# Kernel optimization log

Measured on AMD Instinct MI355X. Metric: run time of the kernel, lower is better.

Reference implementation:

```python
import jax, jax.numpy as jnp
import numpy as np

B, S, D_IN = 2, 2048, 2048
H, G, HD = 16, 4, 128          # num_heads, num_kv_groups, head_dim
GROUP = H // G                  # 4 query heads per kv group
D_OUT = H * HD                  # 2048
EPS = 1e-6


def _rope_tables(seq_len, head_dim, theta=10000.0):
    inv = 1.0 / (theta ** (np.arange(0, head_dim, 2, dtype=np.float32) / head_dim))
    pos = np.arange(seq_len, dtype=np.float32)
    ang = np.outer(pos, inv)                      # [S, HD/2]
    ang = np.concatenate([ang, ang], axis=-1)     # [S, HD]
    return jnp.asarray(np.cos(ang)), jnp.asarray(np.sin(ang))


def setup_inputs() -> dict:
    key = jax.random.key(0)
    ks = jax.random.split(key, 6)
    x = jax.random.normal(ks[0], (B, S, D_IN), dtype=jnp.float32)
    # Linear weights stored as [in, out] so y = x @ W (same math as nn.Linear)
    Wq = jax.random.normal(ks[1], (D_IN, 2 * D_OUT), dtype=jnp.float32) * (D_IN ** -0.5)
    Wk = jax.random.normal(ks[2], (D_IN, G * HD), dtype=jnp.float32) * (D_IN ** -0.5)
    Wv = jax.random.normal(ks[3], (D_IN, G * HD), dtype=jnp.float32) * (D_IN ** -0.5)
    Wo = jax.random.normal(ks[4], (D_OUT, D_IN), dtype=jnp.float32) * (D_OUT ** -0.5)
    q_norm_w = jnp.zeros((HD,), dtype=jnp.float32)  # Qwen-style zero-init (scale = 1 + w)
    k_norm_w = jnp.zeros((HD,), dtype=jnp.float32)
    cos, sin = _rope_tables(S, HD)
    mask = jnp.triu(jnp.ones((S, S), dtype=bool), k=1)  # causal: True above diagonal is masked
    return {"x": x, "Wq": Wq, "Wk": Wk, "Wv": Wv, "Wo": Wo,
            "q_norm_w": q_norm_w, "k_norm_w": k_norm_w,
            "cos": cos, "sin": sin, "mask": mask}


def _rmsnorm(x, w):
    xf = x.astype(jnp.float32)
    n = xf * jax.lax.rsqrt(jnp.mean(xf * xf, axis=-1, keepdims=True) + EPS)
    return (n * (1.0 + w.astype(jnp.float32))).astype(x.dtype)


def _apply_rope(x, cos, sin):
    # x: [..., S, HD]; full-dim rotation (rot_dim == head_dim)
    s = x.shape[-2]
    c = cos[:s][None, None]
    sn = sin[:s][None, None]
    x1, x2 = x[..., : HD // 2], x[..., HD // 2 :]
    rotated = jnp.concatenate([-x2, x1], axis=-1)
    return (x * c + rotated * sn).astype(x.dtype)


def reference(x, Wq, Wk, Wv, Wo, q_norm_w, k_norm_w, cos, sin, mask):
    b, s, _ = x.shape
    qg = (x @ Wq).reshape(b, s, H, 2 * HD)
    q, gate = qg[..., :HD], qg[..., HD:]
    gate = gate.reshape(b, s, D_OUT)
    q = q.transpose(0, 2, 1, 3)                                 # [b,H,s,HD]
    k = (x @ Wk).reshape(b, s, G, HD).transpose(0, 2, 1, 3)     # [b,G,s,HD]
    v = (x @ Wv).reshape(b, s, G, HD).transpose(0, 2, 1, 3)
    q = _rmsnorm(q, q_norm_w)
    k = _rmsnorm(k, k_norm_w)
    q = _apply_rope(q, cos, sin)
    k = _apply_rope(k, cos, sin)
    # GQA: group query heads by kv group instead of repeat_interleave on k/v
    qg4 = q.reshape(b, G, GROUP, s, HD)
    scores = jnp.einsum("bgjqd,bgkd->bgjqk", qg4, k)            # [b,G,GROUP,s,s]
    scores = jnp.where(mask[None, None, None], -jnp.inf, scores)
    w = jax.nn.softmax((scores * (HD ** -0.5)).astype(jnp.float32), axis=-1).astype(q.dtype)
    ctx = jnp.einsum("bgjqk,bgkd->bgjqd", w, v)                 # [b,G,GROUP,s,HD]
    ctx = ctx.reshape(b, H, s, HD).transpose(0, 2, 1, 3).reshape(b, s, D_OUT)
    ctx = ctx * jax.nn.sigmoid(gate)
    return ctx @ Wo
```

## Files before the change

### kernel.cpp

```cpp
#include <hip/hip_runtime.h>

#define S_LEN 2048
#define NROWS 4096
#define DIN   2048
#define DQG   4096
#define DKV   1024

typedef __bf16 bf16x8 __attribute__((ext_vector_type(8)));
typedef float  floatx4 __attribute__((ext_vector_type(4)));
typedef unsigned short u16;

#define QK_SCALE 0.08838834764831845f

__device__ __forceinline__ u16 f2bf(float f) {
  unsigned int u = __float_as_uint(f);
  u += 0x7fffu + ((u >> 16) & 1u);
  return (u16)(u >> 16);
}

__device__ __forceinline__ void gload_lds16(const void* g, void* l) {
  __builtin_amdgcn_global_load_lds(
      (__attribute__((address_space(1))) void*)(void*)(g),
      (__attribute__((address_space(3))) void*)(l), 16, 0, 0);
}

__global__ __launch_bounds__(256) void cvt_f32_bf16(const float* __restrict__ src,
                                                    u16* __restrict__ dst, int n4) {
  int i = blockIdx.x * 256 + threadIdx.x;
  if (i >= n4) return;
  float4 v = reinterpret_cast<const float4*>(src)[i];
  ushort4 o;
  o.x = f2bf(v.x); o.y = f2bf(v.y); o.z = f2bf(v.z); o.w = f2bf(v.w);
  reinterpret_cast<ushort4*>(dst)[i] = o;
}

__global__ __launch_bounds__(256) void tcvt(const float* __restrict__ src,
                                            u16* __restrict__ dst,
                                            int R, int C, int dld) {
  __shared__ float tile[32][33];
  const int c0 = blockIdx.x * 32, r0 = blockIdx.y * 32;
  const int t = threadIdx.x;
  {
    const int rl = t >> 3, cl4 = (t & 7) * 4;
    const float4 v = *reinterpret_cast<const float4*>(src + (size_t)(r0 + rl) * C + c0 + cl4);
    tile[rl][cl4 + 0] = v.x; tile[rl][cl4 + 1] = v.y;
    tile[rl][cl4 + 2] = v.z; tile[rl][cl4 + 3] = v.w;
  }
  __syncthreads();
  {
    const int cl = t >> 3, rl4 = (t & 7) * 4;
    ushort4 o;
    o.x = f2bf(tile[rl4 + 0][cl]); o.y = f2bf(tile[rl4 + 1][cl]);
    o.z = f2bf(tile[rl4 + 2][cl]); o.w = f2bf(tile[rl4 + 3][cl]);
    *reinterpret_cast<ushort4*>(dst + (size_t)(c0 + cl) * dld + r0 + rl4) = o;
  }
}

__global__ __launch_bounds__(256) void gemm_bt(const u16* __restrict__ A,
                                               const u16* __restrict__ Bt,
                                               float* __restrict__ C,
                                               int M, int N, int K) {
  __shared__ __align__(16) u16 As[128 * 32];
  __shared__ __align__(16) u16 Bs[128 * 32];
  const int tid = threadIdx.x, wv = tid >> 6, lane = tid & 63;
  const int m0 = blockIdx.y * 128, n0 = blockIdx.x * 128;
  const int wm = (wv >> 1) * 64, wn = (wv & 1) * 64;
  const int frow = lane & 15, fk = (lane >> 4) * 8;
  const int srow = lane >> 2, skoff = (lane & 3) * 8;
  floatx4 acc[4][4] = {};
  for (int k0 = 0; k0 < K; k0 += 32) {
#pragma unroll
    for (int i = 0; i < 2; ++i) {
      const int rr = (wv * 2 + i) * 16;
      gload_lds16(A  + (size_t)(m0 + rr + srow) * K + k0 + skoff, &As[rr * 32]);
      gload_lds16(Bt + (size_t)(n0 + rr + srow) * K + k0 + skoff, &Bs[rr * 32]);
    }
    __syncthreads();
    bf16x8 af[4], bfr[4];
#pragma unroll
    for (int mi = 0; mi < 4; ++mi)
      af[mi] = *reinterpret_cast<const bf16x8*>(&As[(wm + mi * 16 + frow) * 32 + fk]);
#pragma unroll
    for (int ni = 0; ni < 4; ++ni)
      bfr[ni] = *reinterpret_cast<const bf16x8*>(&Bs[(wn + ni * 16 + frow) * 32 + fk]);
#pragma unroll
    for (int mi = 0; mi < 4; ++mi)
#pragma unroll
      for (int ni = 0; ni < 4; ++ni)
        acc[mi][ni] = __builtin_amdgcn_mfma_f32_16x16x32_bf16(af[mi], bfr[ni], acc[mi][ni], 0, 0, 0);
    __syncthreads();
  }
  const int crow = (lane >> 4) * 4, ccol = lane & 15;
#pragma unroll
  for (int mi = 0; mi < 4; ++mi)
#pragma unroll
    for (int ni = 0; ni < 4; ++ni) {
      float* cp = C + (size_t)(m0 + wm + mi * 16 + crow) * N + (n0 + wn + ni * 16 + ccol);
#pragma unroll
      for (int r = 0; r < 4; ++r) cp[(size_t)r * N] = acc[mi][ni][r];
    }
}

__global__ __launch_bounds__(256) void qnorm_rope(const float* __restrict__ QG,
                                                  const float* __restrict__ w,
                                                  const float* __restrict__ cosT,
                                                  const float* __restrict__ sinT,
                                                  u16* __restrict__ Qb) {
  const int wv = threadIdx.x >> 6, lane = threadIdx.x & 63;
  const int idx = blockIdx.x * 4 + wv;
  const int h = idx & 15, row = idx >> 4;
  const int s = row & (S_LEN - 1), b = row >> 11;
  const float* base = QG + (size_t)row * DQG + h * 256;
  const float v0 = base[lane], v1 = base[lane + 64];
  float ss = v0 * v0 + v1 * v1;
#pragma unroll
  for (int m = 32; m >= 1; m >>= 1) ss += __shfl_xor(ss, m);
  const float rn = rsqrtf(ss * (1.0f / 128.0f) + 1e-6f) * QK_SCALE;
  const float n0 = v0 * rn * (1.0f + w[lane]);
  const float n1 = v1 * rn * (1.0f + w[lane + 64]);
  const float c0 = cosT[(size_t)s * 128 + lane], c1 = cosT[(size_t)s * 128 + lane + 64];
  const float sn0 = sinT[(size_t)s * 128 + lane], sn1 = sinT[(size_t)s * 128 + lane + 64];
  u16* qb = Qb + ((size_t)(b * 16 + h) * S_LEN + s) * 128;
  qb[lane]      = f2bf(n0 * c0 - n1 * sn0);
  qb[lane + 64] = f2bf(n1 * c1 + n0 * sn1);
}

__global__ __launch_bounds__(256) void knorm_rope(const float* __restrict__ KV,
                                                  const float* __restrict__ w,
                                                  const float* __restrict__ cosT,
                                                  const float* __restrict__ sinT,
                                                  u16* __restrict__ Kb) {
  const int wv = threadIdx.x >> 6, lane = threadIdx.x & 63;
  const int idx = blockIdx.x * 4 + wv;
  const int g = idx & 3, row = idx >> 2;
  const int s = row & (S_LEN - 1), b = row >> 11;
  const float* base = KV + (size_t)row * DKV + g * 128;
  const float v0 = base[lane], v1 = base[lane + 64];
  float ss = v0 * v0 + v1 * v1;
#pragma unroll
  for (int m = 32; m >= 1; m >>= 1) ss += __shfl_xor(ss, m);
  const float rn = rsqrtf(ss * (1.0f / 128.0f) + 1e-6f);
  const float n0 = v0 * rn * (1.0f + w[lane]);
  const float n1 = v1 * rn * (1.0f + w[lane + 64]);
  const float c0 = cosT[(size_t)s * 128 + lane], c1 = cosT[(size_t)s * 128 + lane + 64];
  const float sn0 = sinT[(size_t)s * 128 + lane], sn1 = sinT[(size_t)s * 128 + lane + 64];
  u16* kb = Kb + ((size_t)(b * 4 + g) * S_LEN + s) * 128;
  const int sw = s & 7;
  const int d0 = lane, d1 = lane + 64;
  const int p0 = (((d0 >> 3) ^ sw) << 3) | (d0 & 7);
  const int p1 = (((d1 >> 3) ^ sw) << 3) | (d1 & 7);
  kb[p0] = f2bf(n0 * c0 - n1 * sn0);
  kb[p1] = f2bf(n1 * c1 + n0 * sn1);
}

__global__ __launch_bounds__(256) void vtrans(const float* __restrict__ KV,
                                              u16* __restrict__ Vt) {
  __shared__ float tile[32][33];
  const int bg = blockIdx.z;
  const int s0 = blockIdx.x * 32, d0 = blockIdx.y * 32;
  const int b = bg >> 2, g = bg & 3;
  const int t = threadIdx.x;
  {
    const int sl = t >> 3, dl4 = (t & 7) * 4;
    const float4 v = *reinterpret_cast<const float4*>(
        KV + ((size_t)(b * S_LEN + s0 + sl)) * DKV + 512 + g * 128 + d0 + dl4);
    tile[sl][dl4 + 0] = v.x; tile[sl][dl4 + 1] = v.y;
    tile[sl][dl4 + 2] = v.z; tile[sl][dl4 + 3] = v.w;
  }
  __syncthreads();
  {
    const int dl = t >> 3, sl4 = (t & 7) * 4;
    ushort4 o;
    o.x = f2bf(tile[sl4 + 0][dl]); o.y = f2bf(tile[sl4 + 1][dl]);
    o.z = f2bf(tile[sl4 + 2][dl]); o.w = f2bf(tile[sl4 + 3][dl]);
    const int d = d0 + dl, s = s0 + sl4;
    const size_t base = (size_t)(bg * 128 + d) * S_LEN + (s & ~63);
    const int pos = ((((s >> 3) & 7) ^ (d & 7)) << 3) | (s & 7);
    *reinterpret_cast<ushort4*>(Vt + base + pos) = o;
  }
}

__global__ __launch_bounds__(256) void attn(const u16* __restrict__ Qb,
                                            const u16* __restrict__ Kb,
                                            const u16* __restrict__ Vt,
                                            const float* __restrict__ QG,
                                            u16* __restrict__ ctxg) {
  __shared__ __align__(16) u16 Ks[64 * 128];
  __shared__ __align__(16) u16 Vts[128 * 64];
  __shared__ __align__(16) u16 Ps[4][16 * 68];
  const int tid = threadIdx.x, wv = tid >> 6, lane = tid & 63;
  const int ip = blockIdx.x, bh = blockIdx.y;
  const int b = bh >> 4, h = bh & 15, g = h >> 2, bg = b * 4 + g;
  const int f = lane & 15, quad = lane >> 4, fq = quad * 8;
  const int fsw = f & 7;
  const u16* Kp = Kb + (size_t)bg * S_LEN * 128;
  const u16* Vp = Vt + (size_t)bg * 128 * S_LEN;
  u16* Pw = Ps[wv];

  for (int pass = 0; pass < 2; ++pass) {
    const int qt = pass ? 31 - ip : ip;
    const u16* Qp = Qb + ((size_t)bh * S_LEN + qt * 64 + wv * 16) * 128;
    bf16x8 aq[4];
#pragma unroll
    for (int c = 0; c < 4; ++c)
      aq[c] = *reinterpret_cast<const bf16x8*>(&Qp[(size_t)f * 128 + c * 32 + fq]);

    floatx4 o[8] = {};
    float lsum[4] = {0.f, 0.f, 0.f, 0.f};
    const int nkt = qt + 1;

    for (int kt = 0; kt < nkt; ++kt) {
      const int k0 = kt * 64;
#pragma unroll
      for (int i = 0; i < 4; ++i) {
        const int j = wv * 4 + i;
        gload_lds16(Kp + (size_t)k0 * 128 + j * 512 + lane * 8, &Ks[j * 512]);
      }
#pragma unroll
      for (int i = 0; i < 4; ++i) {
        const int r0 = (wv * 4 + i) * 8;
        gload_lds16(Vp + (size_t)(r0 + (lane >> 3)) * S_LEN + k0 + (lane & 7) * 8,
                    &Vts[r0 * 64]);
      }
      __syncthreads();

      floatx4 sc[4] = {};
#pragma unroll
      for (int c = 0; c < 4; ++c) {
#pragma unroll
        for (int n = 0; n < 4; ++n) {
          bf16x8 bk = *reinterpret_cast<const bf16x8*>(
              &Ks[(n * 16 + f) * 128 + (((4 * c + quad) ^ fsw) << 3)]);
          sc[n] = __builtin_amdgcn_mfma_f32_16x16x32_bf16(aq[c], bk, sc[n], 0, 0, 0);
        }
      }

      const int qrow0 = qt * 64 + wv * 16 + quad * 4;
#pragma unroll
      for (int n = 0; n < 4; ++n) {
        const int key = k0 + n * 16 + f;
#pragma unroll
        for (int r = 0; r < 4; ++r) {
          const float p = (key <= qrow0 + r) ? __expf(sc[n][r]) : 0.f;
          lsum[r] += p;
          Pw[(quad * 4 + r) * 68 + n * 16 + f] = f2bf(p);
        }
      }

#pragma unroll
      for (int kf = 0; kf < 2; ++kf) {
        bf16x8 pf = *reinterpret_cast<const bf16x8*>(&Pw[f * 68 + kf * 32 + fq]);
#pragma unroll
        for (int dt = 0; dt < 8; ++dt) {
          bf16x8 bv = *reinterpret_cast<const bf16x8*>(
              &Vts[(dt * 16 + f) * 64 + (((4 * kf + quad) ^ fsw) << 3)]);
          o[dt] = __builtin_amdgcn_mfma_f32_16x16x32_bf16(pf, bv, o[dt], 0, 0, 0);
        }
      }
      __syncthreads();
    }

#pragma unroll
    for (int r = 0; r < 4; ++r) {
#pragma unroll
      for (int mm = 8; mm >= 1; mm >>= 1) lsum[r] += __shfl_xor(lsum[r], mm);
    }

#pragma unroll
    for (int r = 0; r < 4; ++r) {
      const int s = qt * 64 + wv * 16 + quad * 4 + r;
      const size_t grow = (size_t)b * S_LEN + s;
      const float inv = 1.0f / lsum[r];
#pragma unroll
      for (int dt = 0; dt < 8; ++dt) {
        const int d = dt * 16 + f;
        const float gate = QG[grow * DQG + h * 256 + 128 + d];
        const float val = o[dt][r] * inv * (1.0f / (1.0f + __expf(-gate)));
        ctxg[grow * 2048 + h * 128 + d] = f2bf(val);
      }
    }
  }
}

extern "C" void kernel_launch(void* const* d_in, const int* in_sizes, int n_in,
                              void* d_out, int out_size, void* d_ws, size_t ws_size,
                              hipStream_t stream) {
  const float* x    = (const float*)d_in[0];
  const float* Wq   = (const float*)d_in[1];
  const float* Wk   = (const float*)d_in[2];
  const float* Wv   = (const float*)d_in[3];
  const float* Wo   = (const float*)d_in[4];
  const float* qnw  = (const float*)d_in[5];
  const float* knw  = (const float*)d_in[6];
  const float* cosT = (const float*)d_in[7];
  const float* sinT = (const float*)d_in[8];

  char* p = (char*)d_ws;
  u16*   xb   = (u16*)p;  p += (size_t)NROWS * DIN * 2;
  u16*   WqT  = (u16*)p;  p += (size_t)DQG * DIN * 2;
  u16*   WkvT = (u16*)p;  p += (size_t)DKV * DIN * 2;
  u16*   WoT  = (u16*)p;  p += (size_t)2048 * 2048 * 2;
  float* QGf  = (float*)p; p += (size_t)NROWS * DQG * 4;
  float* KVf  = (float*)p; p += (size_t)NROWS * DKV * 4;
  u16*   Qbf  = (u16*)p;  p += (size_t)2 * 16 * S_LEN * 128 * 2;
  u16*   Kbf  = (u16*)p;  p += (size_t)2 * 4 * S_LEN * 128 * 2;
  u16*   Vtb  = (u16*)p;  p += (size_t)2 * 4 * S_LEN * 128 * 2;
  u16*   ctxg = (u16*)p;  p += (size_t)NROWS * 2048 * 2;

  cvt_f32_bf16<<<8192, 256, 0, stream>>>(x, xb, NROWS * DIN / 4);
  tcvt<<<dim3(128, 64), 256, 0, stream>>>(Wq, WqT, 2048, 4096, 2048);
  tcvt<<<dim3(16, 64), 256, 0, stream>>>(Wk, WkvT, 2048, 512, 2048);
  tcvt<<<dim3(16, 64), 256, 0, stream>>>(Wv, WkvT + (size_t)512 * 2048, 2048, 512, 2048);
  tcvt<<<dim3(64, 64), 256, 0, stream>>>(Wo, WoT, 2048, 2048, 2048);

  gemm_bt<<<dim3(32, 32), 256, 0, stream>>>(xb, WqT, QGf, NROWS, DQG, DIN);
  gemm_bt<<<dim3(8, 32), 256, 0, stream>>>(xb, WkvT, KVf, NROWS, DKV, DIN);

  qnorm_rope<<<16384, 256, 0, stream>>>(QGf, qnw, cosT, sinT, Qbf);
  knorm_rope<<<4096, 256, 0, stream>>>(KVf, knw, cosT, sinT, Kbf);
  vtrans<<<dim3(64, 4, 8), 256, 0, stream>>>(KVf, Vtb);

  attn<<<dim3(16, 32), 256, 0, stream>>>(Qbf, Kbf, Vtb, QGf, ctxg);

  gemm_bt<<<dim3(16, 32), 256, 0, stream>>>(ctxg, WoT, (float*)d_out, NROWS, 2048, 2048);
}
```

Measured before the change: 466.8 us.

## Fuse QKV GEMMs, use bf16 intermediates, swizzled 64-wide K tiles in GEMM

```diff
diff --git a/kernel.cpp b/kernel.cpp
--- a/kernel.cpp
+++ b/kernel.cpp
@@ -3,8 +3,8 @@
 #define S_LEN 2048
 #define NROWS 4096
 #define DIN   2048
+#define DQKV  5120
 #define DQG   4096
-#define DKV   1024
 
 typedef __bf16 bf16x8 __attribute__((ext_vector_type(8)));
 typedef float  floatx4 __attribute__((ext_vector_type(4)));
@@ -17,6 +17,12 @@
   u += 0x7fffu + ((u >> 16) & 1u);
   return (u16)(u >> 16);
 }
+__device__ __forceinline__ float bf2f(u16 v) {
+  return __uint_as_float(((unsigned int)v) << 16);
+}
+__device__ __forceinline__ int swz(int col, int row) {
+  return (col & ~63) | ((((col >> 3) & 7) ^ (row & 7)) << 3) | (col & 7);
+}
 
 __device__ __forceinline__ void gload_lds16(const void* g, void* l) {
   __builtin_amdgcn_global_load_lds(
@@ -24,14 +30,14 @@
       (__attribute__((address_space(3))) void*)(l), 16, 0, 0);
 }
 
-__global__ __launch_bounds__(256) void cvt_f32_bf16(const float* __restrict__ src,
-                                                    u16* __restrict__ dst, int n4) {
-  int i = blockIdx.x * 256 + threadIdx.x;
-  if (i >= n4) return;
-  float4 v = reinterpret_cast<const float4*>(src)[i];
+__global__ __launch_bounds__(256) void cvt_x(const float* __restrict__ src,
+                                             u16* __restrict__ dst) {
+  const int i = blockIdx.x * 256 + threadIdx.x;
+  const int row = i >> 9, col = (i & 511) << 2;
+  const float4 v = reinterpret_cast<const float4*>(src)[i];
   ushort4 o;
   o.x = f2bf(v.x); o.y = f2bf(v.y); o.z = f2bf(v.z); o.w = f2bf(v.w);
-  reinterpret_cast<ushort4*>(dst)[i] = o;
+  *reinterpret_cast<ushort4*>(dst + (size_t)row * DIN + swz(col, row)) = o;
 }
 
 __global__ __launch_bounds__(256) void tcvt(const float* __restrict__ src,
@@ -52,42 +58,49 @@
     ushort4 o;
     o.x = f2bf(tile[rl4 + 0][cl]); o.y = f2bf(tile[rl4 + 1][cl]);
     o.z = f2bf(tile[rl4 + 2][cl]); o.w = f2bf(tile[rl4 + 3][cl]);
-    *reinterpret_cast<ushort4*>(dst + (size_t)(c0 + cl) * dld + r0 + rl4) = o;
-  }
-}
-
+    const int rd = c0 + cl, cd = r0 + rl4;
+    *reinterpret_cast<ushort4*>(dst + (size_t)rd * dld + swz(cd, rd)) = o;
+  }
+}
+
+template <bool BF16_OUT>
 __global__ __launch_bounds__(256) void gemm_bt(const u16* __restrict__ A,
                                                const u16* __restrict__ Bt,
-                                               float* __restrict__ C,
+                                               void* __restrict__ Cv,
                                                int M, int N, int K) {
-  __shared__ __align__(16) u16 As[128 * 32];
-  __shared__ __align__(16) u16 Bs[128 * 32];
+  __shared__ __align__(16) u16 As[128 * 64];
+  __shared__ __align__(16) u16 Bs[128 * 64];
   const int tid = threadIdx.x, wv = tid >> 6, lane = tid & 63;
   const int m0 = blockIdx.y * 128, n0 = blockIdx.x * 128;
   const int wm = (wv >> 1) * 64, wn = (wv & 1) * 64;
-  const int frow = lane & 15, fk = (lane >> 4) * 8;
-  const int srow = lane >> 2, skoff = (lane & 3) * 8;
+  const int frow = lane & 15, quad = lane >> 4, fsw = frow & 7;
+  const int srow = lane >> 3, scol = (lane & 7) * 8;
   floatx4 acc[4][4] = {};
-  for (int k0 = 0; k0 < K; k0 += 32) {
-#pragma unroll
-    for (int i = 0; i < 2; ++i) {
-      const int rr = (wv * 2 + i) * 16;
-      gload_lds16(A  + (size_t)(m0 + rr + srow) * K + k0 + skoff, &As[rr * 32]);
-      gload_lds16(Bt + (size_t)(n0 + rr + srow) * K + k0 + skoff, &Bs[rr * 32]);
+  for (int k0 = 0; k0 < K; k0 += 64) {
+#pragma unroll
+    for (int i = 0; i < 4; ++i) {
+      const int rr = (wv * 4 + i) * 8;
+      gload_lds16(A  + (size_t)(m0 + rr + srow) * K + k0 + scol, &As[rr * 64]);
+      gload_lds16(Bt + (size_t)(n0 + rr + srow) * K + k0 + scol, &Bs[rr * 64]);
     }
     __syncthreads();
-    bf16x8 af[4], bfr[4];
-#pragma unroll
-    for (int mi = 0; mi < 4; ++mi)
-      af[mi] = *reinterpret_cast<const bf16x8*>(&As[(wm + mi * 16 + frow) * 32 + fk]);
-#pragma unroll
-    for (int ni = 0; ni < 4; ++ni)
-      bfr[ni] = *reinterpret_cast<const bf16x8*>(&Bs[(wn + ni * 16 + frow) * 32 + fk]);
-#pragma unroll
-    for (int mi = 0; mi < 4; ++mi)
+#pragma unroll
+    for (int ks = 0; ks < 2; ++ks) {
+      bf16x8 af[4], bfr[4];
+#pragma unroll
+      for (int mi = 0; mi < 4; ++mi)
+        af[mi] = *reinterpret_cast<const bf16x8*>(
+            &As[(wm + mi * 16 + frow) * 64 + (((ks * 4 + quad) ^ fsw) << 3)]);
 #pragma unroll
       for (int ni = 0; ni < 4; ++ni)
-        acc[mi][ni] = __builtin_amdgcn_mfma_f32_16x16x32_bf16(af[mi], bfr[ni], acc[mi][ni], 0, 0, 0);
+        bfr[ni] = *reinterpret_cast<const bf16x8*>(
+            &Bs[(wn + ni * 16 + frow) * 64 + (((ks * 4 + quad) ^ fsw) << 3)]);
+#pragma unroll
+      for (int mi = 0; mi < 4; ++mi)
+#pragma unroll
+        for (int ni = 0; ni < 4; ++ni)
+          acc[mi][ni] = __builtin_amdgcn_mfma_f32_16x16x32_bf16(af[mi], bfr[ni], acc[mi][ni], 0, 0, 0);
+    }
     __syncthreads();
   }
   const int crow = (lane >> 4) * 4, ccol = lane & 15;
@@ -95,13 +108,20 @@
   for (int mi = 0; mi < 4; ++mi)
 #pragma unroll
     for (int ni = 0; ni < 4; ++ni) {
-      float* cp = C + (size_t)(m0 + wm + mi * 16 + crow) * N + (n0 + wn + ni * 16 + ccol);
-#pragma unroll
-      for (int r = 0; r < 4; ++r) cp[(size_t)r * N] = acc[mi][ni][r];
-    }
-}
-
-__global__ __launch_bounds__(256) void qnorm_rope(const float* __restrict__ QG,
+      const size_t base = (size_t)(m0 + wm + mi * 16 + crow) * N + (n0 + wn + ni * 16 + ccol);
+      if constexpr (BF16_OUT) {
+        u16* C = (u16*)Cv;
+#pragma unroll
+        for (int r = 0; r < 4; ++r) C[base + (size_t)r * N] = f2bf(acc[mi][ni][r]);
+      } else {
+        float* C = (float*)Cv;
+#pragma unroll
+        for (int r = 0; r < 4; ++r) C[base + (size_t)r * N] = acc[mi][ni][r];
+      }
+    }
+}
+
+__global__ __launch_bounds__(256) void qnorm_rope(const u16* __restrict__ QKV,
                                                   const float* __restrict__ w,
                                                   const float* __restrict__ cosT,
                                                   const float* __restrict__ sinT,
@@ -110,8 +130,8 @@
   const int idx = blockIdx.x * 4 + wv;
   const int h = idx & 15, row = idx >> 4;
   const int s = row & (S_LEN - 1), b = row >> 11;
-  const float* base = QG + (size_t)row * DQG + h * 256;
-  const float v0 = base[lane], v1 = base[lane + 64];
+  const u16* base = QKV + (size_t)row * DQKV + h * 256;
+  const float v0 = bf2f(base[lane]), v1 = bf2f(base[lane + 64]);
   float ss = v0 * v0 + v1 * v1;
 #pragma unroll
   for (int m = 32; m >= 1; m >>= 1) ss += __shfl_xor(ss, m);
@@ -125,7 +145,7 @@
   qb[lane + 64] = f2bf(n1 * c1 + n0 * sn1);
 }
 
-__global__ __launch_bounds__(256) void knorm_rope(const float* __restrict__ KV,
+__global__ __launch_bounds__(256) void knorm_rope(const u16* __restrict__ QKV,
                                                   const float* __restrict__ w,
                                                   const float* __restrict__ cosT,
                                                   const float* __restrict__ sinT,
@@ -134,8 +154,8 @@
   const int idx = blockIdx.x * 4 + wv;
   const int g = idx & 3, row = idx >> 2;
   const int s = row & (S_LEN - 1), b = row >> 11;
-  const float* base = KV + (size_t)row * DKV + g * 128;
-  const float v0 = base[lane], v1 = base[lane + 64];
+  const u16* base = QKV + (size_t)row * DQKV + DQG + g * 128;
+  const float v0 = bf2f(base[lane]), v1 = bf2f(base[lane + 64]);
   float ss = v0 * v0 + v1 * v1;
 #pragma unroll
   for (int m = 32; m >= 1; m >>= 1) ss += __shfl_xor(ss, m);
@@ -153,17 +173,17 @@
   kb[p1] = f2bf(n1 * c1 + n0 * sn1);
 }
 
-__global__ __launch_bounds__(256) void vtrans(const float* __restrict__ KV,
+__global__ __launch_bounds__(256) void vtrans(const u16* __restrict__ QKV,
                                               u16* __restrict__ Vt) {
-  __shared__ float tile[32][33];
+  __shared__ u16 tile[32][40];
   const int bg = blockIdx.z;
   const int s0 = blockIdx.x * 32, d0 = blockIdx.y * 32;
   const int b = bg >> 2, g = bg & 3;
   const int t = threadIdx.x;
   {
     const int sl = t >> 3, dl4 = (t & 7) * 4;
-    const float4 v = *reinterpret_cast<const float4*>(
-        KV + ((size_t)(b * S_LEN + s0 + sl)) * DKV + 512 + g * 128 + d0 + dl4);
+    const ushort4 v = *reinterpret_cast<const ushort4*>(
+        QKV + (size_t)(b * S_LEN + s0 + sl) * DQKV + DQG + 512 + g * 128 + d0 + dl4);
     tile[sl][dl4 + 0] = v.x; tile[sl][dl4 + 1] = v.y;
     tile[sl][dl4 + 2] = v.z; tile[sl][dl4 + 3] = v.w;
   }
@@ -171,8 +191,8 @@
   {
     const int dl = t >> 3, sl4 = (t & 7) * 4;
     ushort4 o;
-    o.x = f2bf(tile[sl4 + 0][dl]); o.y = f2bf(tile[sl4 + 1][dl]);
-    o.z = f2bf(tile[sl4 + 2][dl]); o.w = f2bf(tile[sl4 + 3][dl]);
+    o.x = tile[sl4 + 0][dl]; o.y = tile[sl4 + 1][dl];
+    o.z = tile[sl4 + 2][dl]; o.w = tile[sl4 + 3][dl];
     const int d = d0 + dl, s = s0 + sl4;
     const size_t base = (size_t)(bg * 128 + d) * S_LEN + (s & ~63);
     const int pos = ((((s >> 3) & 7) ^ (d & 7)) << 3) | (s & 7);
@@ -183,7 +203,7 @@
 __global__ __launch_bounds__(256) void attn(const u16* __restrict__ Qb,
                                             const u16* __restrict__ Kb,
                                             const u16* __restrict__ Vt,
-                                            const float* __restrict__ QG,
+                                            const u16* __restrict__ QKV,
                                             u16* __restrict__ ctxg) {
   __shared__ __align__(16) u16 Ks[64 * 128];
   __shared__ __align__(16) u16 Vts[128 * 64];
@@ -274,9 +294,10 @@
 #pragma unroll
       for (int dt = 0; dt < 8; ++dt) {
         const int d = dt * 16 + f;
-        const float gate = QG[grow * DQG + h * 256 + 128 + d];
+        const float gate = bf2f(QKV[grow * DQKV + h * 256 + 128 + d]);
         const float val = o[dt][r] * inv * (1.0f / (1.0f + __expf(-gate)));
-        ctxg[grow * 2048 + h * 128 + d] = f2bf(val);
+        const int col = h * 128 + d;
+        ctxg[grow * 2048 + swz(col, (int)grow)] = f2bf(val);
       }
     }
   }
@@ -296,31 +317,28 @@
   const float* sinT = (const float*)d_in[8];
 
   char* p = (char*)d_ws;
-  u16*   xb   = (u16*)p;  p += (size_t)NROWS * DIN * 2;
-  u16*   WqT  = (u16*)p;  p += (size_t)DQG * DIN * 2;
-  u16*   WkvT = (u16*)p;  p += (size_t)DKV * DIN * 2;
-  u16*   WoT  = (u16*)p;  p += (size_t)2048 * 2048 * 2;
-  float* QGf  = (float*)p; p += (size_t)NROWS * DQG * 4;
-  float* KVf  = (float*)p; p += (size_t)NROWS * DKV * 4;
-  u16*   Qbf  = (u16*)p;  p += (size_t)2 * 16 * S_LEN * 128 * 2;
-  u16*   Kbf  = (u16*)p;  p += (size_t)2 * 4 * S_LEN * 128 * 2;
-  u16*   Vtb  = (u16*)p;  p += (size_t)2 * 4 * S_LEN * 128 * 2;
-  u16*   ctxg = (u16*)p;  p += (size_t)NROWS * 2048 * 2;
-
-  cvt_f32_bf16<<<8192, 256, 0, stream>>>(x, xb, NROWS * DIN / 4);
-  tcvt<<<dim3(128, 64), 256, 0, stream>>>(Wq, WqT, 2048, 4096, 2048);
-  tcvt<<<dim3(16, 64), 256, 0, stream>>>(Wk, WkvT, 2048, 512, 2048);
-  tcvt<<<dim3(16, 64), 256, 0, stream>>>(Wv, WkvT + (size_t)512 * 2048, 2048, 512, 2048);
+  u16*   xb    = (u16*)p;  p += (size_t)NROWS * DIN * 2;
+  u16*   WqkvT = (u16*)p;  p += (size_t)DQKV * DIN * 2;
+  u16*   WoT   = (u16*)p;  p += (size_t)2048 * 2048 * 2;
+  u16*   QKVb  = (u16*)p;  p += (size_t)NROWS * DQKV * 2;
+  u16*   Qbf   = (u16*)p;  p += (size_t)2 * 16 * S_LEN * 128 * 2;
+  u16*   Kbf   = (u16*)p;  p += (size_t)2 * 4 * S_LEN * 128 * 2;
+  u16*   Vtb   = (u16*)p;  p += (size_t)2 * 4 * S_LEN * 128 * 2;
+  u16*   ctxg  = (u16*)p;  p += (size_t)NROWS * 2048 * 2;
+
+  cvt_x<<<8192, 256, 0, stream>>>(x, xb);
+  tcvt<<<dim3(128, 64), 256, 0, stream>>>(Wq, WqkvT, 2048, 4096, 2048);
+  tcvt<<<dim3(16, 64), 256, 0, stream>>>(Wk, WqkvT + (size_t)4096 * 2048, 2048, 512, 2048);
+  tcvt<<<dim3(16, 64), 256, 0, stream>>>(Wv, WqkvT + (size_t)4608 * 2048, 2048, 512, 2048);
   tcvt<<<dim3(64, 64), 256, 0, stream>>>(Wo, WoT, 2048, 2048, 2048);
 
-  gemm_bt<<<dim3(32, 32), 256, 0, stream>>>(xb, WqT, QGf, NROWS, DQG, DIN);
-  gemm_bt<<<dim3(8, 32), 256, 0, stream>>>(xb, WkvT, KVf, NROWS, DKV, DIN);
-
-  qnorm_rope<<<16384, 256, 0, stream>>>(QGf, qnw, cosT, sinT, Qbf);
-  knorm_rope<<<4096, 256, 0, stream>>>(KVf, knw, cosT, sinT, Kbf);
-  vtrans<<<dim3(64, 4, 8), 256, 0, stream>>>(KVf, Vtb);
-
-  attn<<<dim3(16, 32), 256, 0, stream>>>(Qbf, Kbf, Vtb, QGf, ctxg);
-
-  gemm_bt<<<dim3(16, 32), 256, 0, stream>>>(ctxg, WoT, (float*)d_out, NROWS, 2048, 2048);
-}
+  gemm_bt<true><<<dim3(40, 32), 256, 0, stream>>>(xb, WqkvT, QKVb, NROWS, DQKV, DIN);
+
+  qnorm_rope<<<16384, 256, 0, stream>>>(QKVb, qnw, cosT, sinT, Qbf);
+  knorm_rope<<<4096, 256, 0, stream>>>(QKVb, knw, cosT, sinT, Kbf);
+  vtrans<<<dim3(64, 4, 8), 256, 0, stream>>>(QKVb, Vtb);
+
+  attn<<<dim3(16, 32), 256, 0, stream>>>(Qbf, Kbf, Vtb, QKVb, ctxg);
+
+  gemm_bt<false><<<dim3(16, 32), 256, 0, stream>>>(ctxg, WoT, (float*)d_out, NROWS, 2048, 2048);
+}
```

Result: faster. 395.2 us (-15.3%).
